# Optimization experiments

Hardware: AMD Instinct MI355X
Metric: run time of the kernel (lower is better)

Reference implementation:

```python
import jax, jax.numpy as jnp
import numpy as np

N_NODES = 100000
N_EDGES = 1600000
F_IN = 6
HID = 128
GOUT = 64
NUMFEATS = 1024
OUTCHS = 4


def setup_inputs() -> dict:
    key = jax.random.key(0)
    ks = jax.random.split(key, 20)
    s = 0.05
    return {
        "x": jax.random.normal(ks[0], (NUMFEATS,), jnp.float32),
        "node_feat": jax.random.normal(ks[1], (N_NODES, F_IN), jnp.float32),
        "src": jax.random.randint(ks[2], (N_EDGES,), 0, N_NODES),
        "dst": jax.random.randint(ks[3], (N_EDGES,), 0, N_NODES),
        # GraphConv weights (in, out) + bias, DGL convention out = norm_agg(h) @ W + b
        "Wg1": jax.random.normal(ks[4], (F_IN, HID), jnp.float32) * s,
        "bg1": jnp.zeros((HID,), jnp.float32),
        "Wg2": jax.random.normal(ks[5], (HID, HID), jnp.float32) * s,
        "bg2": jnp.zeros((HID,), jnp.float32),
        "Wg3": jax.random.normal(ks[6], (HID, GOUT), jnp.float32) * s,
        "bg3": jnp.zeros((GOUT,), jnp.float32),
        # FC stack (stored as (in, out))
        "W1": jax.random.normal(ks[7], (NUMFEATS, 64), jnp.float32) * s,
        "b1": jnp.zeros((64,), jnp.float32),
        "W2": jax.random.normal(ks[8], (128, 64), jnp.float32) * s,
        "b2": jnp.zeros((64,), jnp.float32),
        "W3": jax.random.normal(ks[9], (64, 32), jnp.float32) * s,
        "b3": jnp.zeros((32,), jnp.float32),
        "W4": jax.random.normal(ks[10], (32, OUTCHS), jnp.float32) * s,
        "b4": jnp.zeros((OUTCHS,), jnp.float32),
    }


def reference(x, node_feat, src, dst,
              Wg1, bg1, Wg2, bg2, Wg3, bg3,
              W1, b1, W2, b2, W3, b3, W4, b4):
    n = node_feat.shape[0]
    # dgl.add_self_loop
    loops = jnp.arange(n, dtype=src.dtype)
    src_ = jnp.concatenate([src, loops])
    dst_ = jnp.concatenate([dst, loops])
    ones = jnp.ones(src_.shape[0], jnp.float32)
    deg_out = jax.ops.segment_sum(ones, src_, num_segments=n)
    deg_in = jax.ops.segment_sum(ones, dst_, num_segments=n)
    c_src = jnp.clip(deg_out, 1.0, None) ** -0.5  # [n]
    c_dst = jnp.clip(deg_in, 1.0, None) ** -0.5   # [n]

    def gconv(h, W, b):
        # DGL GraphConv norm='both': D_in^{-1/2} A D_out^{-1/2} h W + b
        if W.shape[0] > W.shape[1]:
            h = h @ W  # project first when it shrinks messages
        m = (h * c_src[:, None])[src_]                 # [E+n, f]
        agg = jax.ops.segment_sum(m, dst_, num_segments=n)
        agg = agg * c_dst[:, None]
        if W.shape[0] <= W.shape[1]:
            agg = agg @ W
        return agg + b

    h = jax.nn.relu(gconv(node_feat, Wg1, bg1))
    h = jax.nn.relu(gconv(h, Wg2, bg2))
    h = gconv(h, Wg3, bg3)
    graph_state = jnp.mean(h, axis=0)  # dgl.mean_nodes + squeeze -> [GOUT]

    x1 = jax.nn.relu(x @ W1 + b1)                      # [64]
    z = jnp.concatenate([x1, graph_state], axis=0)     # [128]
    z = jax.nn.relu(z @ W2 + b2)
    z = jax.nn.relu(z @ W3 + b3)
    return z @ W4 + b4                                  # [OUTCHS]
```

## Files before the change

kernel.cpp:

```cpp
#include <hip/hip_runtime.h>

#define F_IN 6
#define HID 128
#define GOUT 64
#define SLOT 64
#define BSZ 512
#define EPB 8192
#define NBKT_MAX 256

typedef __attribute__((ext_vector_type(8))) short bf16x8;
typedef __attribute__((ext_vector_type(4))) float f32x4;

__device__ inline float lo2f(unsigned int u) {
  union { unsigned int u; float f; } v; v.u = u << 16; return v.f;
}
__device__ inline float hi2f(unsigned int u) {
  union { unsigned int u; float f; } v; v.u = u & 0xffff0000u; return v.f;
}
__device__ inline unsigned short f2bf(float f) {
  union { float f; unsigned int u; } v; v.f = f;
  unsigned int r = v.u + 0x7fffu + ((v.u >> 16) & 1u);
  return (unsigned short)(r >> 16);
}


__global__ __launch_bounds__(256) void k_hist2(const int* __restrict__ src,
                                               const int* __restrict__ dst,
                                               int* __restrict__ cntD, int* __restrict__ cntS,
                                               int E, int NB) {
  __shared__ int hd[NBKT_MAX], hs[NBKT_MAX];
  int tid = threadIdx.x;
  hd[tid] = 0; hs[tid] = 0;
  __syncthreads();
  int base = blockIdx.x * EPB;
  int end = min(base + EPB, E);
  int e0 = base + tid * 4;
  for (; e0 + 3 < end; e0 += 1024) {
    int4 sv = *(const int4*)(src + e0);
    int4 dv = *(const int4*)(dst + e0);
    atomicAdd(&hd[dv.x >> 9], 1); atomicAdd(&hd[dv.y >> 9], 1);
    atomicAdd(&hd[dv.z >> 9], 1); atomicAdd(&hd[dv.w >> 9], 1);
    atomicAdd(&hs[sv.x >> 9], 1); atomicAdd(&hs[sv.y >> 9], 1);
    atomicAdd(&hs[sv.z >> 9], 1); atomicAdd(&hs[sv.w >> 9], 1);
  }
  for (; e0 < end; ++e0) {
    atomicAdd(&hd[dst[e0] >> 9], 1);
    atomicAdd(&hs[src[e0] >> 9], 1);
  }
  __syncthreads();
  if (tid < NB) {
    cntD[blockIdx.x * NB + tid] = hd[tid];
    cntS[blockIdx.x * NB + tid] = hs[tid];
  }
}

__global__ __launch_bounds__(256) void k_red2w(int* __restrict__ cntD, int* __restrict__ cntS,
                                               int* __restrict__ totD, int* __restrict__ totS,
                                               const float* __restrict__ W2,
                                               uint4* __restrict__ W2p,
                                               int NB, int NBLK) {
  int b = blockIdx.x;
  int tid = threadIdx.x;
  if (b >= 2 * NB) {
    int idx = (b - 2 * NB) * 256 + tid;
    if (idx < 2048) {
      int l = idx & 63, kc = (idx >> 6) & 3, nt = idx >> 8;
      int k0 = kc * 32 + (l >> 4) * 8;
      int c = nt * 16 + (l & 15);
      unsigned short h[8];
#pragma unroll
      for (int e = 0; e < 8; ++e) h[e] = f2bf(W2[(size_t)(k0 + e) * HID + c]);
      uint4 u;
      u.x = (unsigned int)h[0] | ((unsigned int)h[1] << 16);
      u.y = (unsigned int)h[2] | ((unsigned int)h[3] << 16);
      u.z = (unsigned int)h[4] | ((unsigned int)h[5] << 16);
      u.w = (unsigned int)h[6] | ((unsigned int)h[7] << 16);
      W2p[idx] = u;
    }
    return;
  }
  __shared__ int s[256];
  int* cnt; int* tot;
  if (b < NB) { cnt = cntD; tot = totD; } else { cnt = cntS; tot = totS; b -= NB; }
  int own = (tid < NBLK) ? cnt[tid * NB + b] : 0;
  s[tid] = own;
  __syncthreads();
  for (int off = 1; off < 256; off <<= 1) {
    int t = (tid >= off) ? s[tid - off] : 0;
    __syncthreads();
    s[tid] += t;
    __syncthreads();
  }
  if (tid < NBLK) cnt[tid * NB + b] = s[tid] - own;
  if (tid == 255) tot[b] = s[255];
}

__global__ __launch_bounds__(256) void k_base(const int* __restrict__ totD,
                                              const int* __restrict__ totS,
                                              int* __restrict__ bbD, int* __restrict__ bbS,
                                              int NB) {
  __shared__ int s[256];
  int tid = threadIdx.x;
  int own = (tid < NB) ? totD[tid] : 0;
  s[tid] = own;
  __syncthreads();
  for (int off = 1; off < 256; off <<= 1) {
    int t = (tid >= off) ? s[tid - off] : 0;
    __syncthreads();
    s[tid] += t;
    __syncthreads();
  }
  if (tid < NB) bbD[tid] = s[tid] - own;
  if (tid == NB - 1) bbD[NB] = s[tid];
  __syncthreads();
  own = (tid < NB) ? totS[tid] : 0;
  s[tid] = own;
  __syncthreads();
  for (int off = 1; off < 256; off <<= 1) {
    int t = (tid >= off) ? s[tid - off] : 0;
    __syncthreads();
    s[tid] += t;
    __syncthreads();
  }
  if (tid < NB) bbS[tid] = s[tid] - own;
  if (tid == NB - 1) bbS[NB] = s[tid];
}

__global__ __launch_bounds__(256) void k_scat2(const int* __restrict__ src,
                                               const int* __restrict__ dst,
                                               const int* __restrict__ cntD,
                                               const int* __restrict__ cntS,
                                               const int* __restrict__ bbD,
                                               const int* __restrict__ bbS,
                                               unsigned int* __restrict__ packD,
                                               unsigned int* __restrict__ packS,
                                               int E, int NB) {
  __shared__ int curD[NBKT_MAX], curS[NBKT_MAX];
  int tid = threadIdx.x;
  if (tid < NB) {
    curD[tid] = bbD[tid] + cntD[blockIdx.x * NB + tid];
    curS[tid] = bbS[tid] + cntS[blockIdx.x * NB + tid];
  }
  __syncthreads();
  int base = blockIdx.x * EPB;
  int end = min(base + EPB, E);
  int e0 = base + tid * 4;
  for (; e0 + 3 < end; e0 += 1024) {
    int4 sv = *(const int4*)(src + e0);
    int4 dv = *(const int4*)(dst + e0);
    int s4[4] = {sv.x, sv.y, sv.z, sv.w};
    int d4[4] = {dv.x, dv.y, dv.z, dv.w};
#pragma unroll
    for (int k = 0; k < 4; ++k) {
      int pd = atomicAdd(&curD[d4[k] >> 9], 1);
      packD[pd] = ((unsigned int)(d4[k] & 511) << 17) | (unsigned int)s4[k];
      int ps = atomicAdd(&curS[s4[k] >> 9], 1);
      packS[ps] = ((unsigned int)(s4[k] & 511) << 17) | (unsigned int)d4[k];
    }
  }
  for (; e0 < end; ++e0) {
    int s_ = src[e0], d_ = dst[e0];
    int pd = atomicAdd(&curD[d_ >> 9], 1);
    packD[pd] = ((unsigned int)(d_ & 511) << 17) | (unsigned int)s_;
    int ps = atomicAdd(&curS[s_ >> 9], 1);
    packS[ps] = ((unsigned int)(s_ & 511) << 17) | (unsigned int)d_;
  }
}

__global__ __launch_bounds__(256) void k_place(const int* __restrict__ bbD,
                                               const unsigned int* __restrict__ packD,
                                               int* __restrict__ es, int* __restrict__ cursor,
                                               float* __restrict__ cd, int n) {
  __shared__ int cur[BSZ];
  int tid = threadIdx.x;
  for (int i = tid; i < BSZ; i += 256) cur[i] = 0;
  __syncthreads();
  int b = blockIdx.x;
  int lo = bbD[b], hi = bbD[b + 1];
  int nb0 = b << 9;
  for (int j = lo + tid; j < hi; j += 256) {
    unsigned int v = packD[j];
    int s_ = (int)(v & 0x1FFFFu);
    int dl = (int)(v >> 17);
    int k = atomicAdd(&cur[dl], 1);
    es[(size_t)(nb0 + dl) * SLOT + k] = s_;
  }
  __syncthreads();
  for (int i = tid; i < BSZ; i += 256) {
    int node = nb0 + i;
    if (node < n) {
      cursor[node] = node * SLOT + cur[i];
      cd[node] = rsqrtf((float)cur[i] + 1.0f);
    }
  }
}

__global__ __launch_bounds__(256) void k_cntw(const int* __restrict__ bbS,
                                              const unsigned int* __restrict__ packS,
                                              const float* __restrict__ cd,
                                              const float* __restrict__ nf,
                                              float* __restrict__ cs, float* __restrict__ wt,
                                              uint4* __restrict__ nf16, int n) {
  __shared__ int cnt[BSZ];
  __shared__ float wsm[BSZ];
  int tid = threadIdx.x;
  for (int i = tid; i < BSZ; i += 256) { cnt[i] = 0; wsm[i] = 0.f; }
  __syncthreads();
  int b = blockIdx.x;
  int lo = bbS[b], hi = bbS[b + 1];
  int nb0 = b << 9;
  for (int j = lo + tid; j < hi; j += 256) {
    unsigned int v = packS[j];
    int d_ = (int)(v & 0x1FFFFu);
    int sl = (int)(v >> 17);
    atomicAdd(&cnt[sl], 1);
    atomicAdd(&wsm[sl], cd[d_]);
  }
  __syncthreads();
  for (int i = tid; i < BSZ; i += 256) {
    int node = nb0 + i;
    if (node < n) {
      float c_ = rsqrtf((float)cnt[i] + 1.0f);
      cs[node] = c_;
      wt[node] = c_ * (wsm[i] + cd[node]);
      const float2* nf2 = (const float2*)nf + (size_t)node * 3;
      float2 p0 = nf2[0], p1 = nf2[1], p2 = nf2[2];
      uint4 u;
      u.x = (unsigned int)f2bf(p0.x * c_) | ((unsigned int)f2bf(p0.y * c_) << 16);
      u.y = (unsigned int)f2bf(p1.x * c_) | ((unsigned int)f2bf(p1.y * c_) << 16);
      u.z = (unsigned int)f2bf(p2.x * c_) | ((unsigned int)f2bf(p2.y * c_) << 16);
      u.w = 0;
      nf16[node] = u;
    }
  }
}

__global__ __launch_bounds__(256) void k_g6h1(const int* __restrict__ cursor,
                                              const int* __restrict__ es,
                                              const uint4* __restrict__ nf16,
                                              const float* __restrict__ cs,
                                              const float* __restrict__ cd,
                                              const float* __restrict__ Wg1,
                                              const float* __restrict__ bg1,
                                              unsigned char* __restrict__ h1q, int n) {
  __shared__ float vsh[32][6];
  __shared__ float csh[32];
  int tid = threadIdx.x;
  int nl = tid >> 3, l8 = tid & 7;
  int node = blockIdx.x * 32 + nl;
  bool valid = node < n;
  int nodec = valid ? node : 0;
  const int* ep = es + (size_t)nodec * SLOT;
  int esr[8];
#pragma unroll
  for (int k = 0; k < 8; ++k) esr[k] = ep[l8 + 8 * k];
  int deg = valid ? (cursor[node] - node * SLOT) : 0;
  float a0 = 0.f, a1 = 0.f, a2 = 0.f, a3 = 0.f, a4 = 0.f, a5 = 0.f;
#pragma unroll
  for (int k = 0; k < 8; ++k) {
    if (l8 + 8 * k < deg) {
      uint4 u = nf16[esr[k]];
      a0 += lo2f(u.x); a1 += hi2f(u.x);
      a2 += lo2f(u.y); a3 += hi2f(u.y);
      a4 += lo2f(u.z); a5 += hi2f(u.z);
    }
  }
#pragma unroll
  for (int m = 1; m < 8; m <<= 1) {
    a0 += __shfl_xor(a0, m); a1 += __shfl_xor(a1, m); a2 += __shfl_xor(a2, m);
    a3 += __shfl_xor(a3, m); a4 += __shfl_xor(a4, m); a5 += __shfl_xor(a5, m);
  }
  if (valid && l8 == 0) {
    uint4 u = nf16[node];
    float cdi = cd[node];
    vsh[nl][0] = (a0 + lo2f(u.x)) * cdi;
    vsh[nl][1] = (a1 + hi2f(u.x)) * cdi;
    vsh[nl][2] = (a2 + lo2f(u.y)) * cdi;
    vsh[nl][3] = (a3 + hi2f(u.y)) * cdi;
    vsh[nl][4] = (a4 + lo2f(u.z)) * cdi;
    vsh[nl][5] = (a5 + hi2f(u.z)) * cdi;
    csh[nl] = cs[node];
  }
  __syncthreads();
  if (!valid) return;
  int o0 = l8 * 16;
  float v0 = vsh[nl][0], v1 = vsh[nl][1], v2 = vsh[nl][2];
  float v3 = vsh[nl][3], v4 = vsh[nl][4], v5 = vsh[nl][5];
  float csi = csh[nl];
  unsigned int qw[4];
#pragma unroll
  for (int g = 0; g < 4; ++g) {
    unsigned int w_ = 0;
#pragma unroll
    for (int k = 0; k < 4; ++k) {
      int o = o0 + g * 4 + k;
      float acc = bg1[o] + v0 * Wg1[o] + v1 * Wg1[HID + o] + v2 * Wg1[2 * HID + o] +
                  v3 * Wg1[3 * HID + o] + v4 * Wg1[4 * HID + o] + v5 * Wg1[5 * HID + o];
      unsigned int q = (unsigned int)fminf(fmaf(fmaxf(acc, 0.f) * csi, 256.f, 0.5f), 255.f);
      w_ |= q << (k * 8);
    }
    qw[g] = w_;
  }
  *(uint4*)(h1q + (size_t)node * HID + o0) = make_uint4(qw[0], qw[1], qw[2], qw[3]);
}

__global__ __launch_bounds__(512, 8) void k_gh2m(const int* __restrict__ cursor,
                                                 const int* __restrict__ es,
                                                 const unsigned char* __restrict__ h1q,
                                                 const float* __restrict__ cd,
                                                 const uint4* __restrict__ W2p,
                                                 const float* __restrict__ b2,
                                                 const float* __restrict__ wt,
                                                 float* __restrict__ hsumR, int n) {
  __shared__ uint4 Alds[32 * 16];
  __shared__ float hsumL[128];
  int tid = threadIdx.x;
  int w = tid >> 6, l = tid & 63;
  int base = blockIdx.x * 32;
  if (tid < 128) hsumL[tid] = 0.f;
  int rr = l >> 4, fl = l & 15;
  int row = w * 4 + rr;
  int node = base + row;
  bool valid = node < n;
  int nodec = valid ? node : 0;
  const int* ep = es + (size_t)nodec * SLOT;
  int esr0 = ep[fl], esr1 = ep[fl + 16], esr2 = ep[fl + 32], esr3 = ep[fl + 48];
  int deg = valid ? (cursor[node] - node * SLOT) : 0;
  unsigned int a01 = 0, a23 = 0, a45 = 0, a67 = 0;
  const unsigned char* fp = h1q + fl * 8;
  if (valid) {
    uint2 v = *(const uint2*)(fp + (size_t)node * HID);
    a01 += __builtin_amdgcn_perm(0u, v.x, 0x04010400u);
    a23 += __builtin_amdgcn_perm(0u, v.x, 0x04030402u);
    a45 += __builtin_amdgcn_perm(0u, v.y, 0x04010400u);
    a67 += __builtin_amdgcn_perm(0u, v.y, 0x04030402u);
  }
  int srcbase = l & 48;
#define EDGE_BLK(ESK, K)                                                       \
  if (__any(deg > (K) * 16)) {                                                 \
    _Pragma("unroll")                                                          \
    for (int m_ = 0; m_ < 16; ++m_) {                                          \
      if ((K) * 16 + m_ < deg) {                                               \
        int s_ = __shfl(ESK, srcbase | m_);                                    \
        uint2 v_ = *(const uint2*)(fp + (size_t)s_ * HID);                     \
        a01 += __builtin_amdgcn_perm(0u, v_.x, 0x04010400u);                   \
        a23 += __builtin_amdgcn_perm(0u, v_.x, 0x04030402u);                   \
        a45 += __builtin_amdgcn_perm(0u, v_.y, 0x04010400u);                   \
        a67 += __builtin_amdgcn_perm(0u, v_.y, 0x04030402u);                   \
      }                                                                        \
    }                                                                          \
  }
  EDGE_BLK(esr0, 0)
  EDGE_BLK(esr1, 1)
  EDGE_BLK(esr2, 2)
  EDGE_BLK(esr3, 3)
#undef EDGE_BLK
  float m_ = valid ? cd[node] * 0.00390625f : 0.f;
  uint4 u;
  u.x = (unsigned int)f2bf((float)(a01 & 0xffffu) * m_) |
        ((unsigned int)f2bf((float)(a01 >> 16) * m_) << 16);
  u.y = (unsigned int)f2bf((float)(a23 & 0xffffu) * m_) |
        ((unsigned int)f2bf((float)(a23 >> 16) * m_) << 16);
  u.z = (unsigned int)f2bf((float)(a45 & 0xffffu) * m_) |
        ((unsigned int)f2bf((float)(a45 >> 16) * m_) << 16);
  u.w = (unsigned int)f2bf((float)(a67 & 0xffffu) * m_) |
        ((unsigned int)f2bf((float)(a67 >> 16) * m_) << 16);
  Alds[row * 16 + (fl ^ (row & 7))] = u;
  __syncthreads();
  int m16 = l & 15, kq = l >> 4;
  int g = w >> 2, np = w & 3;
  int arow = g * 16 + m16;
  bf16x8 afr[4];
#pragma unroll
  for (int kc = 0; kc < 4; ++kc)
    afr[kc] = *(const bf16x8*)&Alds[arow * 16 + ((kc * 4 + kq) ^ (arow & 7))];
  float wtr[4];
#pragma unroll
  for (int r = 0; r < 4; ++r) {
    int rw = base + g * 16 + kq * 4 + r;
    wtr[r] = (rw < n) ? wt[rw] : 0.f;
  }
#pragma unroll
  for (int jnt = 0; jnt < 2; ++jnt) {
    int nt = np * 2 + jnt;
    f32x4 acc = {0.f, 0.f, 0.f, 0.f};
#pragma unroll
    for (int kc = 0; kc < 4; ++kc) {
      bf16x8 bfr = *(const bf16x8*)&W2p[(nt * 4 + kc) * 64 + l];
      acc = __builtin_amdgcn_mfma_f32_16x16x32_bf16(afr[kc], bfr, acc, 0, 0, 0);
    }
    float bias = b2[nt * 16 + m16];
    float p = 0.f;
#pragma unroll
    for (int r = 0; r < 4; ++r) p += fmaxf(acc[r] + bias, 0.f) * wtr[r];
    p += __shfl_xor(p, 16);
    p += __shfl_xor(p, 32);
    if (kq == 0) atomicAdd(&hsumL[nt * 16 + m16], p);
  }
  __syncthreads();
  if (tid < 128) atomicAdd(&hsumR[(blockIdx.x & 7) * 128 + tid], hsumL[tid]);
}

__global__ __launch_bounds__(256) void k_fcx(const float* __restrict__ x,
                                             const float* __restrict__ W1,
                                             float* __restrict__ z1acc) {
  __shared__ float red[256];
  int tid = threadIdx.x;
  int o = tid & 63, kg = tid >> 6;
  int k0 = blockIdx.x * 64 + kg * 16;
  float acc = 0.f;
#pragma unroll
  for (int i = 0; i < 16; ++i) acc += x[k0 + i] * W1[(size_t)(k0 + i) * 64 + o];
  red[tid] = acc;
  __syncthreads();
  if (tid < 64)
    atomicAdd(&z1acc[o], red[o] + red[o + 64] + red[o + 128] + red[o + 192]);
}

__global__ __launch_bounds__(256) void k_fc2(const float* __restrict__ z1acc,
                                             const float* __restrict__ b1,
                                             const float* __restrict__ hsumR,
                                             const float* __restrict__ Wg3, float inv_n,
                                             const float* __restrict__ bg3,
                                             const float* __restrict__ W2, const float* __restrict__ b2,
                                             const float* __restrict__ W3, const float* __restrict__ b3,
                                             const float* __restrict__ W4, const float* __restrict__ b4,
                                             float* __restrict__ out) {
  __shared__ float hred[128];
  __shared__ float z[128];
  __shared__ float z2[64];
  __shared__ float z3[32];
  __shared__ float red[256];
  int tid = threadIdx.x;
  if (tid < 128) {
    float s = 0.f;
#pragma unroll
    for (int r = 0; r < 8; ++r) s += hsumR[r * 128 + tid];
    hred[tid] = s;
  }
  __syncthreads();
  {
    int c = tid & 63, part = tid >> 6;
    float acc = 0.f;
#pragma unroll
    for (int i = 0; i < 32; ++i) {
      int k = part * 32 + i;
      acc += hred[k] * Wg3[(size_t)k * GOUT + c];
    }
    red[tid] = acc;
  }
  __syncthreads();
  if (tid < 64) {
    z[tid] = fmaxf(z1acc[tid] + b1[tid], 0.f);
    z[64 + tid] = (red[tid] + red[tid + 64] + red[tid + 128] + red[tid + 192]) * inv_n + bg3[tid];
  }
  __syncthreads();
  {
    int o = tid & 63, part = tid >> 6;
    float acc = 0.f;
#pragma unroll
    for (int i = 0; i < 32; ++i) {
      int k = part * 32 + i;
      acc += z[k] * W2[(size_t)k * 64 + o];
    }
    red[tid] = acc;
  }
  __syncthreads();
  if (tid < 64)
    z2[tid] = fmaxf(red[tid] + red[tid + 64] + red[tid + 128] + red[tid + 192] + b2[tid], 0.f);
  __syncthreads();
  {
    int o = tid & 31, part = tid >> 5;
    float acc = 0.f;
#pragma unroll
    for (int i = 0; i < 8; ++i) {
      int k = part * 8 + i;
      acc += z2[k] * W3[(size_t)k * 32 + o];
    }
    red[tid] = acc;
  }
  __syncthreads();
  if (tid < 32) {
    float s = 0.f;
#pragma unroll
    for (int p = 0; p < 8; ++p) s += red[p * 32 + tid];
    z3[tid] = fmaxf(s + b3[tid], 0.f);
  }
  __syncthreads();
  if (tid < 128) {
    int o = tid & 3, part = tid >> 2;
    red[tid] = z3[part] * W4[(size_t)part * 4 + o];
  }
  __syncthreads();
  if (tid < 4) {
    float s = b4[tid];
#pragma unroll
    for (int p = 0; p < 32; ++p) s += red[p * 4 + tid];
    out[tid] = s;
  }
}

extern "C" void kernel_launch(void* const* d_in, const int* in_sizes, int n_in,
                              void* d_out, int out_size, void* d_ws, size_t ws_size,
                              hipStream_t stream) {
  const float* x   = (const float*)d_in[0];
  const float* nf  = (const float*)d_in[1];
  const int*   src = (const int*)d_in[2];
  const int*   dst = (const int*)d_in[3];
  const float* Wg1 = (const float*)d_in[4];
  const float* bg1 = (const float*)d_in[5];
  const float* Wg2 = (const float*)d_in[6];
  const float* bg2 = (const float*)d_in[7];
  const float* Wg3 = (const float*)d_in[8];
  const float* bg3 = (const float*)d_in[9];
  const float* W1  = (const float*)d_in[10];
  const float* b1  = (const float*)d_in[11];
  const float* W2  = (const float*)d_in[12];
  const float* b2  = (const float*)d_in[13];
  const float* W3  = (const float*)d_in[14];
  const float* b3  = (const float*)d_in[15];
  const float* W4  = (const float*)d_in[16];
  const float* b4  = (const float*)d_in[17];

  const int n = in_sizes[1] / F_IN;
  const int E = in_sizes[2];
  const int NB = (n + BSZ - 1) / BSZ;
  const int NBLK = (E + EPB - 1) / EPB;

  char* wsb = (char*)d_ws;
  size_t off = 0;
  auto alloc4 = [&](size_t units) -> void* {
    void* p = wsb + off * 4;
    off += (units + 15) & ~(size_t)15;
    return p;
  };
  float* hsumR  = (float*)alloc4(8 * 128);
  float* z1acc  = (float*)alloc4(64);
  float* cs     = (float*)alloc4(n);
  float* cd     = (float*)alloc4(n);
  float* wt     = (float*)alloc4(n);
  int* cursor   = (int*)alloc4(n);
  int* cntD     = (int*)alloc4((size_t)NBLK * NB);
  int* cntS     = (int*)alloc4((size_t)NBLK * NB);
  int* totD     = (int*)alloc4(NB);
  int* totS     = (int*)alloc4(NB);
  int* bbD      = (int*)alloc4(NB + 1);
  int* bbS      = (int*)alloc4(NB + 1);
  unsigned int* packD = (unsigned int*)alloc4(E);
  unsigned int* packS = (unsigned int*)alloc4(E);
  int* es       = (int*)alloc4((size_t)n * SLOT);
  uint4* nf16   = (uint4*)alloc4((size_t)4 * n);
  unsigned char* h1q = (unsigned char*)alloc4((size_t)32 * n);
  uint4* W2p    = (uint4*)alloc4(2048 * 4);
  (void)ws_size; (void)n_in; (void)out_size;

  hipMemsetAsync(hsumR, 0, (8 * 128 + 64) * sizeof(float), stream);

  k_hist2<<<NBLK, 256, 0, stream>>>(src, dst, cntD, cntS, E, NB);
  k_red2w<<<2 * NB + 8, 256, 0, stream>>>(cntD, cntS, totD, totS, Wg2, W2p, NB, NBLK);
  k_base<<<1, 256, 0, stream>>>(totD, totS, bbD, bbS, NB);
  k_scat2<<<NBLK, 256, 0, stream>>>(src, dst, cntD, cntS, bbD, bbS, packD, packS, E, NB);
  k_place<<<NB, 256, 0, stream>>>(bbD, packD, es, cursor, cd, n);
  k_cntw<<<NB, 256, 0, stream>>>(bbS, packS, cd, nf, cs, wt, nf16, n);

  k_g6h1<<<(n + 31) / 32, 256, 0, stream>>>(cursor, es, nf16, cs, cd, Wg1, bg1, h1q, n);
  k_gh2m<<<(n + 31) / 32, 512, 0, stream>>>(cursor, es, h1q, cd, W2p, bg2, wt, hsumR, n);

  k_fcx<<<16, 256, 0, stream>>>(x, W1, z1acc);
  k_fc2<<<1, 256, 0, stream>>>(z1acc, b1, hsumR, Wg3, 1.0f / (float)n, bg3,
                               W2, b2, W3, b3, W4, b4, (float*)d_out);
}
```

Measured before the change: 170.5 us.

## Batch gather loads in layer-2 aggregation and shrink edge-per-block bucket size

In the layer-2 gather kernel, each group of 16 neighbor loads is issued into a register buffer before any accumulation, so more memory requests are in flight per wave. The occupancy hint is lowered from 8 to 4 to leave room for the extra registers. Edges per bucketing block drop from 8192 to 2048, which creates more blocks. The prefix-scan kernel now handles 4 entries per thread to cover the larger block count. The trade-off is lower occupancy and more scan work in exchange for more memory-level parallelism and finer-grained bucketing.

```diff
diff --git a/kernel.cpp b/kernel.cpp
--- a/kernel.cpp
+++ b/kernel.cpp
@@ -5,7 +5,7 @@
 #define GOUT 64
 #define SLOT 64
 #define BSZ 512
-#define EPB 8192
+#define EPB 2048
 #define NBKT_MAX 256
 
 typedef __attribute__((ext_vector_type(8))) short bf16x8;
@@ -82,8 +82,15 @@
   __shared__ int s[256];
   int* cnt; int* tot;
   if (b < NB) { cnt = cntD; tot = totD; } else { cnt = cntS; tot = totS; b -= NB; }
-  int own = (tid < NBLK) ? cnt[tid * NB + b] : 0;
-  s[tid] = own;
+  int v[4], sum = 0;
+#pragma unroll
+  for (int k = 0; k < 4; ++k) {
+    int idx = tid * 4 + k;
+    int d = (idx < NBLK) ? cnt[idx * NB + b] : 0;
+    v[k] = sum;
+    sum += d;
+  }
+  s[tid] = sum;
   __syncthreads();
   for (int off = 1; off < 256; off <<= 1) {
     int t = (tid >= off) ? s[tid - off] : 0;
@@ -91,7 +98,12 @@
     s[tid] += t;
     __syncthreads();
   }
-  if (tid < NBLK) cnt[tid * NB + b] = s[tid] - own;
+  int texcl = s[tid] - sum;
+#pragma unroll
+  for (int k = 0; k < 4; ++k) {
+    int idx = tid * 4 + k;
+    if (idx < NBLK) cnt[idx * NB + b] = texcl + v[k];
+  }
   if (tid == 255) tot[b] = s[255];
 }
 
@@ -304,7 +316,7 @@
   *(uint4*)(h1q + (size_t)node * HID + o0) = make_uint4(qw[0], qw[1], qw[2], qw[3]);
 }
 
-__global__ __launch_bounds__(512, 8) void k_gh2m(const int* __restrict__ cursor,
+__global__ __launch_bounds__(512, 4) void k_gh2m(const int* __restrict__ cursor,
                                                  const int* __restrict__ es,
                                                  const unsigned char* __restrict__ h1q,
                                                  const float* __restrict__ cd,
@@ -338,16 +350,21 @@
   int srcbase = l & 48;
 #define EDGE_BLK(ESK, K)                                                       \
   if (__any(deg > (K) * 16)) {                                                 \
+    uint2 vb[16];                                                              \
     _Pragma("unroll")                                                          \
     for (int m_ = 0; m_ < 16; ++m_) {                                          \
+      vb[m_] = make_uint2(0u, 0u);                                             \
       if ((K) * 16 + m_ < deg) {                                               \
         int s_ = __shfl(ESK, srcbase | m_);                                    \
-        uint2 v_ = *(const uint2*)(fp + (size_t)s_ * HID);                     \
-        a01 += __builtin_amdgcn_perm(0u, v_.x, 0x04010400u);                   \
-        a23 += __builtin_amdgcn_perm(0u, v_.x, 0x04030402u);                   \
-        a45 += __builtin_amdgcn_perm(0u, v_.y, 0x04010400u);                   \
-        a67 += __builtin_amdgcn_perm(0u, v_.y, 0x04030402u);                   \
+        vb[m_] = *(const uint2*)(fp + (size_t)s_ * HID);                       \
       }                                                                        \
+    }                                                                          \
+    _Pragma("unroll")                                                          \
+    for (int m_ = 0; m_ < 16; ++m_) {                                          \
+      a01 += __builtin_amdgcn_perm(0u, vb[m_].x, 0x04010400u);                 \
+      a23 += __builtin_amdgcn_perm(0u, vb[m_].x, 0x04030402u);                 \
+      a45 += __builtin_amdgcn_perm(0u, vb[m_].y, 0x04010400u);                 \
+      a67 += __builtin_amdgcn_perm(0u, vb[m_].y, 0x04030402u);                 \
     }                                                                          \
   }
   EDGE_BLK(esr0, 0)
```

Measured after the change: 153.4 us. 10.0% less time.
